# Optimization experiments

Hardware: AMD Instinct MI355X
Metric: run time of the kernel (lower is better)

## Reference

```python
import jax, jax.numpy as jnp
import numpy as np

B = 64
D = 4096          # width of every layer
# DAG: layer k consumes concat of prior layer outputs listed here (0 = input x)
CONNECTIONS = {1: [0], 2: [0, 1], 3: [1, 2], 4: [2, 3]}


def setup_inputs() -> dict:
    key = jax.random.key(0)
    keys = iter(jax.random.split(key, 32))
    inp = {"x": jax.random.normal(next(keys), (B, D), dtype=jnp.float32)}
    for k, v in CONNECTIONS.items():
        fan_in = D * len(v)
        bound = 1.0 / np.sqrt(fan_in)
        # kaiming_uniform_(a=sqrt(5)) -> U(-sqrt(6/((1+5)*fan_in)), +) = U(-1/sqrt(fan_in), +)
        inp[f"W{k}"] = jax.random.uniform(next(keys), (D, fan_in), jnp.float32, -bound, bound)
        inp[f"b{k}"] = jax.random.uniform(next(keys), (D,), jnp.float32, -bound, bound)
        # static binary mask (buffer in torch), stored as float like MaskedLinear expects
        inp[f"M{k}"] = (jax.random.uniform(next(keys), (D, fan_in)) < 0.5).astype(jnp.float32)
    return inp


def _dag_forward(x, Ws, bs, Ms):
    layer_output = [x]
    for k, v in CONNECTIONS.items():
        inputs = jnp.concatenate([layer_output[v_] for v_ in v], axis=1)  # [B, D*len(v)]
        # masked linear: y = inputs @ (W*M)^T + b, then ReLU
        y = jnp.einsum('bi,oi->bo', inputs, Ws[k] * Ms[k]) + bs[k]
        layer_output.append(jax.nn.relu(y))
    return layer_output[-1]


def reference(x, W1, b1, M1, W2, b2, M2, W3, b3, M3, W4, b4, M4):
    Ws = {1: W1, 2: W2, 3: W3, 4: W4}
    bs = {1: b1, 2: b2, 3: b3, 4: b4}
    Ms = {1: M1, 2: M2, 3: M3, 4: M4}
    return _dag_forward(x, Ws, bs, Ms)
```

## Files before the change

### kernel.cpp

```cpp
#include <hip/hip_runtime.h>
#include <hip/hip_bf16.h>
#include <stdint.h>


typedef __attribute__((ext_vector_type(8))) short  s8v;
typedef __attribute__((ext_vector_type(4))) float  f4v;
typedef __attribute__((ext_vector_type(4))) unsigned short us4v;

#define LDA 16384
#define MFMA16x16x32 __builtin_amdgcn_mfma_f32_16x16x32_bf16

__device__ __forceinline__ short f2bf(float f) {
  unsigned int u = __builtin_bit_cast(unsigned int, f);
  u += 0x7fffu + ((u >> 16) & 1u);
  return (short)(u >> 16);
}
__device__ __forceinline__ float bf2f(short s) {
  unsigned int u = ((unsigned int)(unsigned short)s) << 16;
  return __builtin_bit_cast(float, u);
}

__global__ void dag_splitx(const float* __restrict__ x,
                           ushort* __restrict__ xh, ushort* __restrict__ xl) {
  int idx = blockIdx.x * blockDim.x + threadIdx.x;
  int m = idx >> 10;
  int n = (idx & 1023) << 2;
  f4v v = *(const f4v*)(x + (size_t)m * 4096 + n);
  us4v h, l;
#pragma unroll
  for (int j = 0; j < 4; ++j) {
    short hh = f2bf(v[j]);
    h[j] = (unsigned short)hh;
    l[j] = (unsigned short)f2bf(v[j] - bf2f(hh));
  }
  *(us4v*)(xh + (size_t)m * LDA + n) = h;
  *(us4v*)(xl + (size_t)m * LDA + n) = l;
}

__global__ __launch_bounds__(256, 2) void dag_gemm_phaseA(
    const ushort* __restrict__ Ah,
    const ushort* __restrict__ Al,
    const float*  __restrict__ W,
    const float*  __restrict__ Mm,
    float*        __restrict__ partial,
    int K, int klen) {
  const int tid  = threadIdx.x;
  const int wave = tid >> 6, lane = tid & 63;
  const int l15  = lane & 15, blk = lane >> 4;
  const int n0   = blockIdx.x * 128 + wave * 32;
  const int kbeg = blockIdx.y * klen;

  const float* wp0 = W  + (size_t)(n0 + l15) * K + kbeg + blk * 8;
  const float* wp1 = wp0 + (size_t)16 * K;
  const float* mp0 = Mm + (size_t)(n0 + l15) * K + kbeg + blk * 8;
  const float* mp1 = mp0 + (size_t)16 * K;
  const ushort* ap  = Ah + (size_t)l15 * LDA + kbeg + blk * 8;
  const ushort* alp = Al + (size_t)l15 * LDA + kbeg + blk * 8;

  f4v acc[4][2];
#pragma unroll
  for (int i = 0; i < 4; ++i) {
    acc[i][0] = (f4v){0.f, 0.f, 0.f, 0.f};
    acc[i][1] = (f4v){0.f, 0.f, 0.f, 0.f};
  }

  struct R {
    f4v w0a, w0b, w1a, w1b, m0a, m0b, m1a, m1b;
    s8v ah0, ah1, ah2, ah3, al0, al1, al2, al3;
  } r0, r1;

  auto LOAD = [&](R& r, int ko) {
    r.w0a = *(const f4v*)(wp0 + ko);      r.w0b = *(const f4v*)(wp0 + ko + 4);
    r.w1a = *(const f4v*)(wp1 + ko);      r.w1b = *(const f4v*)(wp1 + ko + 4);
    r.m0a = *(const f4v*)(mp0 + ko);      r.m0b = *(const f4v*)(mp0 + ko + 4);
    r.m1a = *(const f4v*)(mp1 + ko);      r.m1b = *(const f4v*)(mp1 + ko + 4);
    r.ah0 = *(const s8v*)(ap  + ko);
    r.ah1 = *(const s8v*)(ap  + (size_t)16 * LDA + ko);
    r.ah2 = *(const s8v*)(ap  + (size_t)32 * LDA + ko);
    r.ah3 = *(const s8v*)(ap  + (size_t)48 * LDA + ko);
    r.al0 = *(const s8v*)(alp + ko);
    r.al1 = *(const s8v*)(alp + (size_t)16 * LDA + ko);
    r.al2 = *(const s8v*)(alp + (size_t)32 * LDA + ko);
    r.al3 = *(const s8v*)(alp + (size_t)48 * LDA + ko);
  };

  auto STEP = [&](R& r) {
    s8v wh0, wl0, wh1, wl1;
#pragma unroll
    for (int j = 0; j < 4; ++j) {
      { float w = r.w0a[j] * r.m0a[j]; short h = f2bf(w);
        wh0[j]     = h; wl0[j]     = f2bf(w - bf2f(h)); }
      { float w = r.w0b[j] * r.m0b[j]; short h = f2bf(w);
        wh0[j + 4] = h; wl0[j + 4] = f2bf(w - bf2f(h)); }
      { float w = r.w1a[j] * r.m1a[j]; short h = f2bf(w);
        wh1[j]     = h; wl1[j]     = f2bf(w - bf2f(h)); }
      { float w = r.w1b[j] * r.m1b[j]; short h = f2bf(w);
        wh1[j + 4] = h; wl1[j + 4] = f2bf(w - bf2f(h)); }
    }
    acc[0][0] = MFMA16x16x32(r.ah0, wh0, acc[0][0], 0, 0, 0);
    acc[0][0] = MFMA16x16x32(r.al0, wh0, acc[0][0], 0, 0, 0);
    acc[0][0] = MFMA16x16x32(r.ah0, wl0, acc[0][0], 0, 0, 0);
    acc[1][0] = MFMA16x16x32(r.ah1, wh0, acc[1][0], 0, 0, 0);
    acc[1][0] = MFMA16x16x32(r.al1, wh0, acc[1][0], 0, 0, 0);
    acc[1][0] = MFMA16x16x32(r.ah1, wl0, acc[1][0], 0, 0, 0);
    acc[2][0] = MFMA16x16x32(r.ah2, wh0, acc[2][0], 0, 0, 0);
    acc[2][0] = MFMA16x16x32(r.al2, wh0, acc[2][0], 0, 0, 0);
    acc[2][0] = MFMA16x16x32(r.ah2, wl0, acc[2][0], 0, 0, 0);
    acc[3][0] = MFMA16x16x32(r.ah3, wh0, acc[3][0], 0, 0, 0);
    acc[3][0] = MFMA16x16x32(r.al3, wh0, acc[3][0], 0, 0, 0);
    acc[3][0] = MFMA16x16x32(r.ah3, wl0, acc[3][0], 0, 0, 0);
    acc[0][1] = MFMA16x16x32(r.ah0, wh1, acc[0][1], 0, 0, 0);
    acc[0][1] = MFMA16x16x32(r.al0, wh1, acc[0][1], 0, 0, 0);
    acc[0][1] = MFMA16x16x32(r.ah0, wl1, acc[0][1], 0, 0, 0);
    acc[1][1] = MFMA16x16x32(r.ah1, wh1, acc[1][1], 0, 0, 0);
    acc[1][1] = MFMA16x16x32(r.al1, wh1, acc[1][1], 0, 0, 0);
    acc[1][1] = MFMA16x16x32(r.ah1, wl1, acc[1][1], 0, 0, 0);
    acc[2][1] = MFMA16x16x32(r.ah2, wh1, acc[2][1], 0, 0, 0);
    acc[2][1] = MFMA16x16x32(r.al2, wh1, acc[2][1], 0, 0, 0);
    acc[2][1] = MFMA16x16x32(r.ah2, wl1, acc[2][1], 0, 0, 0);
    acc[3][1] = MFMA16x16x32(r.ah3, wh1, acc[3][1], 0, 0, 0);
    acc[3][1] = MFMA16x16x32(r.al3, wh1, acc[3][1], 0, 0, 0);
    acc[3][1] = MFMA16x16x32(r.ah3, wl1, acc[3][1], 0, 0, 0);
  };

  const int nsteps = klen >> 5;
  LOAD(r0, 0);
  int ko = 0;
  for (int s = 0; s < nsteps; s += 2) {
    LOAD(r1, ko + 32);
    STEP(r0);
    if (s + 2 < nsteps) LOAD(r0, ko + 64);
    STEP(r1);
    ko += 64;
  }

  float* pout = partial + (size_t)blockIdx.y * (64 * 4096);
#pragma unroll
  for (int mt = 0; mt < 4; ++mt)
#pragma unroll
    for (int nt = 0; nt < 2; ++nt) {
      int n = n0 + nt * 16 + l15;
#pragma unroll
      for (int rr = 0; rr < 4; ++rr) {
        int m = mt * 16 + blk * 4 + rr;
        pout[(size_t)m * 4096 + n] = acc[mt][nt][rr];
      }
    }
}

__global__ void dag_phaseB(const float* __restrict__ partial, int splitk,
                           const float* __restrict__ bias,
                           ushort* __restrict__ yh, ushort* __restrict__ yl,
                           float* __restrict__ yf) {
  int idx = blockIdx.x * blockDim.x + threadIdx.x;
  int m = idx >> 10;
  int n = (idx & 1023) << 2;
  const float* p = partial + (size_t)m * 4096 + n;
  f4v s = (f4v){0.f, 0.f, 0.f, 0.f};
  for (int sp = 0; sp < splitk; ++sp)
    s += *(const f4v*)(p + (size_t)sp * (64 * 4096));
  const f4v bv = *(const f4v*)(bias + n);
  f4v y;
#pragma unroll
  for (int j = 0; j < 4; ++j) y[j] = fmaxf(s[j] + bv[j], 0.f);
  if (yf) *(f4v*)(yf + (size_t)m * 4096 + n) = y;
  if (yh) {
    us4v h, l;
#pragma unroll
    for (int j = 0; j < 4; ++j) {
      short hh = f2bf(y[j]);
      h[j] = (unsigned short)hh;
      l[j] = (unsigned short)f2bf(y[j] - bf2f(hh));
    }
    *(us4v*)(yh + (size_t)m * LDA + n) = h;
    *(us4v*)(yl + (size_t)m * LDA + n) = l;
  }
}

extern "C" void kernel_launch(void* const* d_in, const int* in_sizes, int n_in,
                              void* d_out, int out_size, void* d_ws, size_t ws_size,
                              hipStream_t stream) {
  (void)in_sizes; (void)n_in; (void)out_size;
  const float* x = (const float*)d_in[0];
  struct L { const float *W, *b, *M; int K, incol, outcol; };
  L Ls[4] = {
      {(const float*)d_in[1],  (const float*)d_in[2],  (const float*)d_in[3],  4096, 0,    4096},
      {(const float*)d_in[4],  (const float*)d_in[5],  (const float*)d_in[6],  8192, 0,    8192},
      {(const float*)d_in[7],  (const float*)d_in[8],  (const float*)d_in[9],  8192, 4096, 12288},
      {(const float*)d_in[10], (const float*)d_in[11], (const float*)d_in[12], 8192, 8192, 16384},
  };
  float* out = (float*)d_out;

  char* ws = (char*)d_ws;
  ushort* Ah = (ushort*)ws;
  ushort* Al = (ushort*)(ws + (size_t)64 * LDA * 2);
  float* partial = (float*)(ws + (size_t)2 * 64 * LDA * 2);
  int SPLITK = 16;
  while (SPLITK > 1 &&
         ws_size < (size_t)4 * 1024 * 1024 + (size_t)SPLITK * 1024 * 1024)
    SPLITK >>= 1;

  dag_splitx<<<256, 256, 0, stream>>>(x, Ah, Al);

  for (int k = 0; k < 4; ++k) {
    dim3 grid(32, SPLITK);
    dag_gemm_phaseA<<<grid, 256, 0, stream>>>(
        Ah + Ls[k].incol, Al + Ls[k].incol, Ls[k].W, Ls[k].M, partial,
        Ls[k].K, Ls[k].K / SPLITK);
    bool last = (k == 3);
    dag_phaseB<<<256, 256, 0, stream>>>(
        partial, SPLITK, Ls[k].b,
        last ? (ushort*)nullptr : Ah + Ls[k].outcol,
        last ? (ushort*)nullptr : Al + Ls[k].outcol,
        last ? out : (float*)nullptr);
  }
}
```

Measured before the change: 299.4 us.

## Fuse all DAG layers into one cooperative persistent kernel with grid syncs

Replaces the nine separate launches (x split, then a GEMM and a reduce kernel per layer) with a single cooperative kernel of 512 blocks. Grid-wide barriers separate the input split, each layer's split-K GEMM and its bias+ReLU reduction. The aim is to remove launch gaps and kernel boundary drains between dependent phases. The cost is grid.sync overhead, which matters most at small split-K. If the cooperative launch fails, the code falls back to the old multi-kernel path.

```diff
diff --git a/kernel.cpp b/kernel.cpp
--- a/kernel.cpp
+++ b/kernel.cpp
@@ -1,14 +1,19 @@
 #include <hip/hip_runtime.h>
 #include <hip/hip_bf16.h>
+#include <hip/hip_cooperative_groups.h>
 #include <stdint.h>
+
+namespace cg = cooperative_groups;
 
 
 typedef __attribute__((ext_vector_type(8))) short  s8v;
 typedef __attribute__((ext_vector_type(4))) float  f4v;
+typedef __attribute__((ext_vector_type(2))) float  f2v;
 typedef __attribute__((ext_vector_type(4))) unsigned short us4v;
+typedef __attribute__((ext_vector_type(2))) unsigned short us2v;
 
 #define LDA 16384
-#define MFMA16x16x32 __builtin_amdgcn_mfma_f32_16x16x32_bf16
+#define MFMA16 __builtin_amdgcn_mfma_f32_16x16x32_bf16
 
 __device__ __forceinline__ short f2bf(float f) {
   unsigned int u = __builtin_bit_cast(unsigned int, f);
@@ -18,6 +23,186 @@
 __device__ __forceinline__ float bf2f(short s) {
   unsigned int u = ((unsigned int)(unsigned short)s) << 16;
   return __builtin_bit_cast(float, u);
+}
+
+struct DagArgs {
+  const float* x;
+  const float* W[4];
+  const float* b[4];
+  const float* M[4];
+  float* out;
+  ushort* Ah;
+  ushort* Al;
+  float* partial;
+  int splitk;
+};
+
+__global__ __launch_bounds__(256, 2) void dag_fused(DagArgs P) {
+  cg::grid_group gg = cg::this_grid();
+  const int tid  = threadIdx.x;
+  const int bid  = blockIdx.x;
+  const int gtid = bid * 256 + tid;
+  const int wave = tid >> 6, lane = tid & 63;
+  const int l15  = lane & 15, blk = lane >> 4;
+
+  {
+    int m = gtid >> 11;
+    int n = (gtid & 2047) << 1;
+    f2v v = *(const f2v*)(P.x + (size_t)m * 4096 + n);
+    us2v h, l;
+#pragma unroll
+    for (int j = 0; j < 2; ++j) {
+      short hh = f2bf(v[j]);
+      h[j] = (unsigned short)hh;
+      l[j] = (unsigned short)f2bf(v[j] - bf2f(hh));
+    }
+    *(us2v*)(P.Ah + (size_t)m * LDA + n) = h;
+    *(us2v*)(P.Al + (size_t)m * LDA + n) = l;
+  }
+  gg.sync();
+
+  const int Ks[4]     = {4096, 8192, 8192, 8192};
+  const int incol[4]  = {0, 0, 4096, 8192};
+  const int outcol[4] = {4096, 8192, 12288, 16384};
+
+#pragma unroll 1
+  for (int L = 0; L < 4; ++L) {
+    const int K = Ks[L];
+    const int kb = bid >> 5;
+    if (kb < P.splitk) {
+      const int klen = K / P.splitk;
+      const int kbeg = kb * klen;
+      const int n0   = (bid & 31) * 128 + wave * 32;
+      const float*  Wl  = P.W[L];
+      const float*  Ml  = P.M[L];
+      const ushort* Ahp = P.Ah + incol[L];
+      const ushort* Alp = P.Al + incol[L];
+
+      const float* wp0 = Wl + (size_t)(n0 + l15) * K + kbeg + blk * 8;
+      const float* wp1 = wp0 + (size_t)16 * K;
+      const float* mp0 = Ml + (size_t)(n0 + l15) * K + kbeg + blk * 8;
+      const float* mp1 = mp0 + (size_t)16 * K;
+      const ushort* ap  = Ahp + (size_t)l15 * LDA + kbeg + blk * 8;
+      const ushort* alp = Alp + (size_t)l15 * LDA + kbeg + blk * 8;
+
+      f4v acc[4][2];
+#pragma unroll
+      for (int i = 0; i < 4; ++i) {
+        acc[i][0] = (f4v){0.f, 0.f, 0.f, 0.f};
+        acc[i][1] = (f4v){0.f, 0.f, 0.f, 0.f};
+      }
+
+      struct R {
+        f4v w0a, w0b, w1a, w1b, m0a, m0b, m1a, m1b;
+        s8v ah0, ah1, ah2, ah3, al0, al1, al2, al3;
+      } r0, r1;
+
+      auto LOAD = [&](R& r, int ko) {
+        r.w0a = *(const f4v*)(wp0 + ko);     r.w0b = *(const f4v*)(wp0 + ko + 4);
+        r.w1a = *(const f4v*)(wp1 + ko);     r.w1b = *(const f4v*)(wp1 + ko + 4);
+        r.m0a = *(const f4v*)(mp0 + ko);     r.m0b = *(const f4v*)(mp0 + ko + 4);
+        r.m1a = *(const f4v*)(mp1 + ko);     r.m1b = *(const f4v*)(mp1 + ko + 4);
+        r.ah0 = *(const s8v*)(ap  + ko);
+        r.ah1 = *(const s8v*)(ap  + (size_t)16 * LDA + ko);
+        r.ah2 = *(const s8v*)(ap  + (size_t)32 * LDA + ko);
+        r.ah3 = *(const s8v*)(ap  + (size_t)48 * LDA + ko);
+        r.al0 = *(const s8v*)(alp + ko);
+        r.al1 = *(const s8v*)(alp + (size_t)16 * LDA + ko);
+        r.al2 = *(const s8v*)(alp + (size_t)32 * LDA + ko);
+        r.al3 = *(const s8v*)(alp + (size_t)48 * LDA + ko);
+      };
+
+      auto STEP = [&](R& r) {
+        s8v wh0, wl0, wh1, wl1;
+#pragma unroll
+        for (int j = 0; j < 4; ++j) {
+          { float w = r.w0a[j] * r.m0a[j]; short h = f2bf(w);
+            wh0[j]     = h; wl0[j]     = f2bf(w - bf2f(h)); }
+          { float w = r.w0b[j] * r.m0b[j]; short h = f2bf(w);
+            wh0[j + 4] = h; wl0[j + 4] = f2bf(w - bf2f(h)); }
+          { float w = r.w1a[j] * r.m1a[j]; short h = f2bf(w);
+            wh1[j]     = h; wl1[j]     = f2bf(w - bf2f(h)); }
+          { float w = r.w1b[j] * r.m1b[j]; short h = f2bf(w);
+            wh1[j + 4] = h; wl1[j + 4] = f2bf(w - bf2f(h)); }
+        }
+        acc[0][0] = MFMA16(r.ah0, wh0, acc[0][0], 0, 0, 0);
+        acc[0][0] = MFMA16(r.al0, wh0, acc[0][0], 0, 0, 0);
+        acc[0][0] = MFMA16(r.ah0, wl0, acc[0][0], 0, 0, 0);
+        acc[1][0] = MFMA16(r.ah1, wh0, acc[1][0], 0, 0, 0);
+        acc[1][0] = MFMA16(r.al1, wh0, acc[1][0], 0, 0, 0);
+        acc[1][0] = MFMA16(r.ah1, wl0, acc[1][0], 0, 0, 0);
+        acc[2][0] = MFMA16(r.ah2, wh0, acc[2][0], 0, 0, 0);
+        acc[2][0] = MFMA16(r.al2, wh0, acc[2][0], 0, 0, 0);
+        acc[2][0] = MFMA16(r.ah2, wl0, acc[2][0], 0, 0, 0);
+        acc[3][0] = MFMA16(r.ah3, wh0, acc[3][0], 0, 0, 0);
+        acc[3][0] = MFMA16(r.al3, wh0, acc[3][0], 0, 0, 0);
+        acc[3][0] = MFMA16(r.ah3, wl0, acc[3][0], 0, 0, 0);
+        acc[0][1] = MFMA16(r.ah0, wh1, acc[0][1], 0, 0, 0);
+        acc[0][1] = MFMA16(r.al0, wh1, acc[0][1], 0, 0, 0);
+        acc[0][1] = MFMA16(r.ah0, wl1, acc[0][1], 0, 0, 0);
+        acc[1][1] = MFMA16(r.ah1, wh1, acc[1][1], 0, 0, 0);
+        acc[1][1] = MFMA16(r.al1, wh1, acc[1][1], 0, 0, 0);
+        acc[1][1] = MFMA16(r.ah1, wl1, acc[1][1], 0, 0, 0);
+        acc[2][1] = MFMA16(r.ah2, wh1, acc[2][1], 0, 0, 0);
+        acc[2][1] = MFMA16(r.al2, wh1, acc[2][1], 0, 0, 0);
+        acc[2][1] = MFMA16(r.ah2, wl1, acc[2][1], 0, 0, 0);
+        acc[3][1] = MFMA16(r.ah3, wh1, acc[3][1], 0, 0, 0);
+        acc[3][1] = MFMA16(r.al3, wh1, acc[3][1], 0, 0, 0);
+        acc[3][1] = MFMA16(r.ah3, wl1, acc[3][1], 0, 0, 0);
+      };
+
+      const int nsteps = klen >> 5;
+      LOAD(r0, 0);
+      int ko = 0;
+      for (int s = 0; s < nsteps; s += 2) {
+        LOAD(r1, ko + 32);
+        STEP(r0);
+        if (s + 2 < nsteps) LOAD(r0, ko + 64);
+        STEP(r1);
+        ko += 64;
+      }
+
+      float* pout = P.partial + (size_t)kb * (64 * 4096);
+#pragma unroll
+      for (int mt = 0; mt < 4; ++mt)
+#pragma unroll
+        for (int nt = 0; nt < 2; ++nt) {
+          int n = n0 + nt * 16 + l15;
+#pragma unroll
+          for (int rr = 0; rr < 4; ++rr) {
+            int m = mt * 16 + blk * 4 + rr;
+            pout[(size_t)m * 4096 + n] = acc[mt][nt][rr];
+          }
+        }
+    }
+    gg.sync();
+
+    {
+      int m = gtid >> 11;
+      int n = (gtid & 2047) << 1;
+      const float* p = P.partial + (size_t)m * 4096 + n;
+      float s0 = 0.f, s1 = 0.f;
+      for (int sp = 0; sp < P.splitk; ++sp) {
+        f2v v = *(const f2v*)(p + (size_t)sp * (64 * 4096));
+        s0 += v[0]; s1 += v[1];
+      }
+      f2v bv = *(const f2v*)(P.b[L] + n);
+      s0 = fmaxf(s0 + bv[0], 0.f);
+      s1 = fmaxf(s1 + bv[1], 0.f);
+      if (L == 3) {
+        *(f2v*)(P.out + (size_t)m * 4096 + n) = (f2v){s0, s1};
+      } else {
+        us2v h, l;
+        short h0 = f2bf(s0); h[0] = (unsigned short)h0;
+        l[0] = (unsigned short)f2bf(s0 - bf2f(h0));
+        short h1 = f2bf(s1); h[1] = (unsigned short)h1;
+        l[1] = (unsigned short)f2bf(s1 - bf2f(h1));
+        *(us2v*)(P.Ah + (size_t)m * LDA + outcol[L] + n) = h;
+        *(us2v*)(P.Al + (size_t)m * LDA + outcol[L] + n) = l;
+      }
+    }
+    if (L < 3) gg.sync();
+  }
 }
 
 __global__ void dag_splitx(const float* __restrict__ x,
@@ -38,12 +223,9 @@
 }
 
 __global__ __launch_bounds__(256, 2) void dag_gemm_phaseA(
-    const ushort* __restrict__ Ah,
-    const ushort* __restrict__ Al,
-    const float*  __restrict__ W,
-    const float*  __restrict__ Mm,
-    float*        __restrict__ partial,
-    int K, int klen) {
+    const ushort* __restrict__ Ah, const ushort* __restrict__ Al,
+    const float* __restrict__ W, const float* __restrict__ Mm,
+    float* __restrict__ partial, int K, int klen) {
   const int tid  = threadIdx.x;
   const int wave = tid >> 6, lane = tid & 63;
   const int l15  = lane & 15, blk = lane >> 4;
@@ -63,17 +245,15 @@
     acc[i][0] = (f4v){0.f, 0.f, 0.f, 0.f};
     acc[i][1] = (f4v){0.f, 0.f, 0.f, 0.f};
   }
-
   struct R {
     f4v w0a, w0b, w1a, w1b, m0a, m0b, m1a, m1b;
     s8v ah0, ah1, ah2, ah3, al0, al1, al2, al3;
   } r0, r1;
-
   auto LOAD = [&](R& r, int ko) {
-    r.w0a = *(const f4v*)(wp0 + ko);      r.w0b = *(const f4v*)(wp0 + ko + 4);
-    r.w1a = *(const f4v*)(wp1 + ko);      r.w1b = *(const f4v*)(wp1 + ko + 4);
-    r.m0a = *(const f4v*)(mp0 + ko);      r.m0b = *(const f4v*)(mp0 + ko + 4);
-    r.m1a = *(const f4v*)(mp1 + ko);      r.m1b = *(const f4v*)(mp1 + ko + 4);
+    r.w0a = *(const f4v*)(wp0 + ko);     r.w0b = *(const f4v*)(wp0 + ko + 4);
+    r.w1a = *(const f4v*)(wp1 + ko);     r.w1b = *(const f4v*)(wp1 + ko + 4);
+    r.m0a = *(const f4v*)(mp0 + ko);     r.m0b = *(const f4v*)(mp0 + ko + 4);
+    r.m1a = *(const f4v*)(mp1 + ko);     r.m1b = *(const f4v*)(mp1 + ko + 4);
     r.ah0 = *(const s8v*)(ap  + ko);
     r.ah1 = *(const s8v*)(ap  + (size_t)16 * LDA + ko);
     r.ah2 = *(const s8v*)(ap  + (size_t)32 * LDA + ko);
@@ -83,7 +263,6 @@
     r.al2 = *(const s8v*)(alp + (size_t)32 * LDA + ko);
     r.al3 = *(const s8v*)(alp + (size_t)48 * LDA + ko);
   };
-
   auto STEP = [&](R& r) {
     s8v wh0, wl0, wh1, wl1;
 #pragma unroll
@@ -97,32 +276,31 @@
       { float w = r.w1b[j] * r.m1b[j]; short h = f2bf(w);
         wh1[j + 4] = h; wl1[j + 4] = f2bf(w - bf2f(h)); }
     }
-    acc[0][0] = MFMA16x16x32(r.ah0, wh0, acc[0][0], 0, 0, 0);
-    acc[0][0] = MFMA16x16x32(r.al0, wh0, acc[0][0], 0, 0, 0);
-    acc[0][0] = MFMA16x16x32(r.ah0, wl0, acc[0][0], 0, 0, 0);
-    acc[1][0] = MFMA16x16x32(r.ah1, wh0, acc[1][0], 0, 0, 0);
-    acc[1][0] = MFMA16x16x32(r.al1, wh0, acc[1][0], 0, 0, 0);
-    acc[1][0] = MFMA16x16x32(r.ah1, wl0, acc[1][0], 0, 0, 0);
-    acc[2][0] = MFMA16x16x32(r.ah2, wh0, acc[2][0], 0, 0, 0);
-    acc[2][0] = MFMA16x16x32(r.al2, wh0, acc[2][0], 0, 0, 0);
-    acc[2][0] = MFMA16x16x32(r.ah2, wl0, acc[2][0], 0, 0, 0);
-    acc[3][0] = MFMA16x16x32(r.ah3, wh0, acc[3][0], 0, 0, 0);
-    acc[3][0] = MFMA16x16x32(r.al3, wh0, acc[3][0], 0, 0, 0);
-    acc[3][0] = MFMA16x16x32(r.ah3, wl0, acc[3][0], 0, 0, 0);
-    acc[0][1] = MFMA16x16x32(r.ah0, wh1, acc[0][1], 0, 0, 0);
-    acc[0][1] = MFMA16x16x32(r.al0, wh1, acc[0][1], 0, 0, 0);
-    acc[0][1] = MFMA16x16x32(r.ah0, wl1, acc[0][1], 0, 0, 0);
-    acc[1][1] = MFMA16x16x32(r.ah1, wh1, acc[1][1], 0, 0, 0);
-    acc[1][1] = MFMA16x16x32(r.al1, wh1, acc[1][1], 0, 0, 0);
-    acc[1][1] = MFMA16x16x32(r.ah1, wl1, acc[1][1], 0, 0, 0);
-    acc[2][1] = MFMA16x16x32(r.ah2, wh1, acc[2][1], 0, 0, 0);
-    acc[2][1] = MFMA16x16x32(r.al2, wh1, acc[2][1], 0, 0, 0);
-    acc[2][1] = MFMA16x16x32(r.ah2, wl1, acc[2][1], 0, 0, 0);
-    acc[3][1] = MFMA16x16x32(r.ah3, wh1, acc[3][1], 0, 0, 0);
-    acc[3][1] = MFMA16x16x32(r.al3, wh1, acc[3][1], 0, 0, 0);
-    acc[3][1] = MFMA16x16x32(r.ah3, wl1, acc[3][1], 0, 0, 0);
+    acc[0][0] = MFMA16(r.ah0, wh0, acc[0][0], 0, 0, 0);
+    acc[0][0] = MFMA16(r.al0, wh0, acc[0][0], 0, 0, 0);
+    acc[0][0] = MFMA16(r.ah0, wl0, acc[0][0], 0, 0, 0);
+    acc[1][0] = MFMA16(r.ah1, wh0, acc[1][0], 0, 0, 0);
+    acc[1][0] = MFMA16(r.al1, wh0, acc[1][0], 0, 0, 0);
+    acc[1][0] = MFMA16(r.ah1, wl0, acc[1][0], 0, 0, 0);
+    acc[2][0] = MFMA16(r.ah2, wh0, acc[2][0], 0, 0, 0);
+    acc[2][0] = MFMA16(r.al2, wh0, acc[2][0], 0, 0, 0);
+    acc[2][0] = MFMA16(r.ah2, wl0, acc[2][0], 0, 0, 0);
+    acc[3][0] = MFMA16(r.ah3, wh0, acc[3][0], 0, 0, 0);
+    acc[3][0] = MFMA16(r.al3, wh0, acc[3][0], 0, 0, 0);
+    acc[3][0] = MFMA16(r.ah3, wl0, acc[3][0], 0, 0, 0);
+    acc[0][1] = MFMA16(r.ah0, wh1, acc[0][1], 0, 0, 0);
+    acc[0][1] = MFMA16(r.al0, wh1, acc[0][1], 0, 0, 0);
+    acc[0][1] = MFMA16(r.ah0, wl1, acc[0][1], 0, 0, 0);
+    acc[1][1] = MFMA16(r.ah1, wh1, acc[1][1], 0, 0, 0);
+    acc[1][1] = MFMA16(r.al1, wh1, acc[1][1], 0, 0, 0);
+    acc[1][1] = MFMA16(r.ah1, wl1, acc[1][1], 0, 0, 0);
+    acc[2][1] = MFMA16(r.ah2, wh1, acc[2][1], 0, 0, 0);
+    acc[2][1] = MFMA16(r.al2, wh1, acc[2][1], 0, 0, 0);
+    acc[2][1] = MFMA16(r.ah2, wl1, acc[2][1], 0, 0, 0);
+    acc[3][1] = MFMA16(r.ah3, wh1, acc[3][1], 0, 0, 0);
+    acc[3][1] = MFMA16(r.al3, wh1, acc[3][1], 0, 0, 0);
+    acc[3][1] = MFMA16(r.ah3, wl1, acc[3][1], 0, 0, 0);
   };
-
   const int nsteps = klen >> 5;
   LOAD(r0, 0);
   int ko = 0;
@@ -133,7 +311,6 @@
     STEP(r1);
     ko += 64;
   }
-
   float* pout = partial + (size_t)blockIdx.y * (64 * 4096);
 #pragma unroll
   for (int mt = 0; mt < 4; ++mt)
@@ -200,18 +377,27 @@
          ws_size < (size_t)4 * 1024 * 1024 + (size_t)SPLITK * 1024 * 1024)
     SPLITK >>= 1;
 
-  dag_splitx<<<256, 256, 0, stream>>>(x, Ah, Al);
-
-  for (int k = 0; k < 4; ++k) {
-    dim3 grid(32, SPLITK);
-    dag_gemm_phaseA<<<grid, 256, 0, stream>>>(
-        Ah + Ls[k].incol, Al + Ls[k].incol, Ls[k].W, Ls[k].M, partial,
-        Ls[k].K, Ls[k].K / SPLITK);
-    bool last = (k == 3);
-    dag_phaseB<<<256, 256, 0, stream>>>(
-        partial, SPLITK, Ls[k].b,
-        last ? (ushort*)nullptr : Ah + Ls[k].outcol,
-        last ? (ushort*)nullptr : Al + Ls[k].outcol,
-        last ? out : (float*)nullptr);
-  }
-}
+  DagArgs ha;
+  ha.x = x;
+  for (int k = 0; k < 4; ++k) { ha.W[k] = Ls[k].W; ha.b[k] = Ls[k].b; ha.M[k] = Ls[k].M; }
+  ha.out = out; ha.Ah = Ah; ha.Al = Al; ha.partial = partial; ha.splitk = SPLITK;
+  void* kargs[] = {(void*)&ha};
+
+  hipError_t e = hipLaunchCooperativeKernel((const void*)dag_fused, dim3(512),
+                                            dim3(256), kargs, 0, stream);
+  if (e != hipSuccess) {
+    dag_splitx<<<256, 256, 0, stream>>>(x, Ah, Al);
+    for (int k = 0; k < 4; ++k) {
+      dim3 grid(32, SPLITK);
+      dag_gemm_phaseA<<<grid, 256, 0, stream>>>(
+          Ah + Ls[k].incol, Al + Ls[k].incol, Ls[k].W, Ls[k].M, partial,
+          Ls[k].K, Ls[k].K / SPLITK);
+      bool last = (k == 3);
+      dag_phaseB<<<256, 256, 0, stream>>>(
+          partial, SPLITK, Ls[k].b,
+          last ? (ushort*)nullptr : Ah + Ls[k].outcol,
+          last ? (ushort*)nullptr : Al + Ls[k].outcol,
+          last ? out : (float*)nullptr);
+    }
+  }
+}
```

Measured after the change: 753.5 us. 2.52x slower.
